# Optimization experiments

Measured on AMD Instinct MI355X. Metric: run time of the kernel, lower is better.

## Reference

```python
import jax, jax.numpy as jnp
import numpy as np

TAU = 2.0      # LIF membrane time constant (spikingjelly default-style, decay_input=True)
VTH = 0.5      # v_threshold from init
S = 4          # time_steps
EPS = 1e-5     # BatchNorm eps
ALPHA = 4.0    # surrogate sigmoid alpha (spikingjelly Sigmoid default)

@jax.custom_vjp
def spike(x):
    # Heaviside forward (spikingjelly: x >= 0 -> 1)
    return (x >= 0.0).astype(x.dtype)

def _spike_fwd(x):
    return spike(x), x

def _spike_bwd(x, g):
    sg = jax.nn.sigmoid(ALPHA * x)
    return (g * ALPHA * sg * (1.0 - sg),)

spike.defvjp(_spike_fwd, _spike_bwd)

def bn(y, gamma, beta, mean, var):
    # inference-mode BatchNorm2d over channel axis 1; y: (B, C, T, V)
    inv = gamma * jax.lax.rsqrt(var + EPS)
    return y * inv[None, :, None, None] + (beta - mean * inv)[None, :, None, None]


def setup_inputs() -> dict:
    key = jax.random.key(0)
    ks = jax.random.split(key, 16)
    B, T, C, V, H, NC = 16, 512, 3, 16, 128, 12
    inp = {
        "x": jax.random.normal(ks[0], (B, T, C, V), dtype=jnp.float32),
        "w1": jax.random.normal(ks[1], (H, C), dtype=jnp.float32) * (1.0 / np.sqrt(C)),
        "b1": jax.random.normal(ks[2], (H,), dtype=jnp.float32) * 0.01,
        "g1": jnp.ones((H,), jnp.float32),
        "be1": jnp.zeros((H,), jnp.float32),
        "m1": jax.random.normal(ks[3], (H,), dtype=jnp.float32) * 0.1,
        "rv1": jax.random.uniform(ks[4], (H,), dtype=jnp.float32) + 0.5,
        "w2": jax.random.normal(ks[5], (H, H), dtype=jnp.float32) * (1.0 / np.sqrt(H)),
        "b2": jax.random.normal(ks[6], (H,), dtype=jnp.float32) * 0.01,
        "g2": jnp.ones((H,), jnp.float32),
        "be2": jnp.zeros((H,), jnp.float32),
        "m2": jax.random.normal(ks[7], (H,), dtype=jnp.float32) * 0.1,
        "rv2": jax.random.uniform(ks[8], (H,), dtype=jnp.float32) + 0.5,
        "wc": jax.random.normal(ks[9], (NC, H), dtype=jnp.float32) * (1.0 / np.sqrt(H)),
        "bc": jax.random.normal(ks[10], (NC,), dtype=jnp.float32) * 0.01,
    }
    return inp


def reference(x, w1, b1, g1, be1, m1, rv1, w2, b2, g2, be2, m2, rv2, wc, bc):
    # x: (B, T, C, V) -> channels-first (B, C, T, V) as in torch permute
    xc = jnp.transpose(x, (0, 2, 1, 3))
    # fc1 1x1 conv + BN; input identical across all S steps, so compute once
    h1 = bn(jnp.einsum('bctv,oc->botv', xc, w1) + b1[None, :, None, None],
            g1, be1, m1, rv1)  # (B, H, T, V)

    def step(carry, _):
        v1s, v2s, acc = carry
        # LIF1: decay_input=True, v_reset=0 hard reset
        v1n = v1s + (h1 - v1s) / TAU
        s1 = spike(v1n - VTH)
        v1n = v1n * (1.0 - s1)
        # fc2 1x1 conv + BN on spikes
        h2 = bn(jnp.einsum('botv,po->bptv', s1, w2) + b2[None, :, None, None],
                g2, be2, m2, rv2)
        # LIF2
        v2n = v2s + (h2 - v2s) / TAU
        s2 = spike(v2n - VTH)
        v2n = v2n * (1.0 - s2)
        return (v1n, v2n, acc + s2), None

    z = jnp.zeros_like(h1)
    (_, _, acc), _ = jax.lax.scan(step, (z, z, z), None, length=S)
    # mean over S, then mean over T and V -> (B, H); dropout is identity in eval
    feat = (acc / S).mean(axis=(2, 3))
    return feat @ wc.T + bc
```

## Files before the change

kernel.cpp:

```cpp
#include <hip/hip_runtime.h>
#include <hip/hip_bf16.h>
#include <stdint.h>
#include <math.h>

#define B_ 16
#define T_ 512
#define V_ 16
#define H_ 128
#define NC_ 12

typedef float v2f __attribute__((ext_vector_type(2)));
typedef __attribute__((ext_vector_type(8))) short s8frag;
typedef __attribute__((ext_vector_type(16))) float f16frag;
typedef unsigned long long u64;


__device__ __forceinline__ unsigned short bf16_rne(float w) {
    unsigned u = __float_as_uint(w);
    unsigned r = (u + 0x7FFFu + ((u >> 16) & 1u)) >> 16;
    return (unsigned short)r;
}
__device__ __forceinline__ float bf16_f32(unsigned short h) {
    return __uint_as_float((unsigned)h << 16);
}
__device__ __forceinline__ void split8(const float* __restrict__ s, s8frag& hi, s8frag& lo) {
    #pragma unroll
    for (int j = 0; j < 8; ++j) {
        float w = s[j];
        unsigned short hb = bf16_rne(w);
        unsigned short lb = bf16_rne(w - bf16_f32(hb));
        hi[j] = (short)hb;
        lo[j] = (short)lb;
    }
}
__device__ __forceinline__ uint4 expand8(unsigned bt) {
    uint4 r;
    r.x = ((bt      & 1u) * 0x3F80u) | (((bt >> 1) & 1u) * 0x3F800000u);
    r.y = (((bt >> 2) & 1u) * 0x3F80u) | (((bt >> 3) & 1u) * 0x3F800000u);
    r.z = (((bt >> 4) & 1u) * 0x3F80u) | (((bt >> 5) & 1u) * 0x3F800000u);
    r.w = (((bt >> 6) & 1u) * 0x3F80u) | (((bt >> 7) & 1u) * 0x3F800000u);
    return r;
}

#define ROUNDS 8
__global__ __launch_bounds__(256, 3) void snn_main(
    const float* __restrict__ x,
    const float* __restrict__ w1, const float* __restrict__ b1,
    const float* __restrict__ g1, const float* __restrict__ be1,
    const float* __restrict__ m1, const float* __restrict__ rv1,
    const float* __restrict__ w2, const float* __restrict__ b2,
    const float* __restrict__ g2, const float* __restrict__ be2,
    const float* __restrict__ m2, const float* __restrict__ rv2,
    float* __restrict__ feat)
{
    __shared__ uint4 afrag[2][2][8][64];
    __shared__ uint4 msk[4][16];

    const int tid  = threadIdx.x;
    const int lane = tid & 63;
    const int wv   = tid >> 6;
    const int nl   = lane & 15;
    const int kg   = (lane >> 4) & 1;
    const int ch4  = lane >> 5;
    const int bb   = blockIdx.x >> 6;
    const int sbase = (blockIdx.x & 63) * (ROUNDS * 16);

    const int p = lane, q = lane + 64;
    v2f w0v = { w1[p*3+0], w1[q*3+0] };
    v2f w1v = { w1[p*3+1], w1[q*3+1] };
    v2f w2v = { w1[p*3+2], w1[q*3+2] };
    v2f b1v = { b1[p], b1[q] };
    float i1a = g1[p] * (float)(1.0 / sqrt((double)(rv1[p] + 1e-5f)));
    float i1b = g1[q] * (float)(1.0 / sqrt((double)(rv1[q] + 1e-5f)));
    v2f i1v = { i1a, i1b };
    v2f d1v = { be1[p] - m1[p] * i1a, be1[q] - m1[q] * i1b };

    const int chn = wv * 32 + (lane & 31);
    float i2c = g2[chn] * (float)(1.0 / sqrt((double)(rv2[chn] + 1e-5f)));
    float d2c = be2[chn] - m2[chn] * i2c;
    float b2c = b2[chn];

    s8frag bh[8], bl[8];
    #pragma unroll
    for (int c = 0; c < 8; ++c)
        split8(&w2[chn * H_ + c * 16 + ch4 * 8], bh[c], bl[c]);

    float facc = 0.f;

    #define CONSUME(BUF)                                                        \
        for (int tt = 0; tt < 2; ++tt) {                                        \
            f16frag acch = {0.f,0.f,0.f,0.f,0.f,0.f,0.f,0.f,                    \
                            0.f,0.f,0.f,0.f,0.f,0.f,0.f,0.f};                   \
            f16frag accl = acch;                                                \
            _Pragma("unroll")                                                   \
            for (int c = 0; c < 8; ++c) {                                       \
                s8frag a = *(const s8frag*)&afrag[BUF][tt][c][lane];            \
                acch = __builtin_amdgcn_mfma_f32_32x32x16_bf16(a, bh[c], acch, 0,0,0); \
                accl = __builtin_amdgcn_mfma_f32_32x32x16_bf16(a, bl[c], accl, 0,0,0); \
            }                                                                   \
            f16frag accs = acch + accl;                                         \
            _Pragma("unroll")                                                   \
            for (int g = 0; g < 4; ++g) {                                       \
                float v = 0.f;                                                  \
                _Pragma("unroll")                                               \
                for (int s = 0; s < 4; ++s) {                                   \
                    float h2 = (accs[g*4+s] + b2c) * i2c + d2c;                 \
                    v = v + (h2 - v) * 0.5f;                                    \
                    bool sp = v >= 0.5f;                                        \
                    v = sp ? 0.f : v;                                           \
                    facc += sp ? 1.f : 0.f;                                     \
                }                                                               \
            }                                                                   \
        }

    for (int r = 0; r < ROUNDS; ++r) {
        #pragma unroll
        for (int i = 0; i < 4; ++i) {
            int site = sbase + r * 16 + wv * 4 + i;
            int t = site >> 4, v = site & 15;
            const float* xp = x + ((size_t)(bb * T_ + t) * 3) * V_ + v;
            float x0 = xp[0], x1 = xp[V_], x2 = xp[2 * V_];

            v2f h1 = ((x0 * w0v + x1 * w1v + x2 * w2v) + b1v) * i1v + d1v;
            v2f v1t = h1 * 0.5f;
            v2f v2t = v1t + h1 * 0.25f;
            v2f v3t = v2t + (h1 - v2t) * 0.5f;
            v2f v4t = v3t + (h1 - v3t) * 0.5f;

            u64 t1a = __ballot(v1t.x >= 0.5f), t2a = __ballot(v2t.x >= 0.5f);
            u64 t3a = __ballot(v3t.x >= 0.5f), t4a = __ballot(v4t.x >= 0.5f);
            u64 t1b = __ballot(v1t.y >= 0.5f), t2b = __ballot(v2t.y >= 0.5f);
            u64 t3b = __ballot(v3t.y >= 0.5f), t4b = __ballot(v4t.y >= 0.5f);
            u64 s3a = t1a | (t3a & ~t2a), s3b = t1b | (t3b & ~t2b);
            u64 s4a = t2a | (t4a & ~t3a), s4b = t2b | (t4b & ~t3b);

            u64 mx = (lane == 0) ? t1a : (lane == 1) ? t2a : (lane == 2) ? s3a : s4a;
            u64 my = (lane == 0) ? t1b : (lane == 1) ? t2b : (lane == 2) ? s3b : s4b;
            if (lane < 4) {
                uint4 mm;
                mm.x = (unsigned)mx; mm.y = (unsigned)(mx >> 32);
                mm.z = (unsigned)my; mm.w = (unsigned)(my >> 32);
                msk[wv][i * 4 + lane] = mm;
            }
        }
        {
            uint4 mm = msk[wv][nl];
            u64 wsel = ch4 ? ((u64)mm.z | ((u64)mm.w << 32))
                           : ((u64)mm.x | ((u64)mm.y << 32));
            int tt   = wv >> 1;
            int slot = ((wv & 1) * 16 + nl) + 32 * kg;
            int buf  = r & 1;
            #pragma unroll
            for (int j = 0; j < 4; ++j) {
                unsigned by = (unsigned)(wsel >> (kg * 8 + j * 16)) & 0xFFu;
                afrag[buf][tt][ch4 * 4 + j][slot] = expand8(by);
            }
        }
        if (r > 0) { int pb = (r - 1) & 1; CONSUME(pb); }
        __syncthreads();
    }
    { int pb = (ROUNDS - 1) & 1; CONSUME(pb); }
    #undef CONSUME

    facc += __shfl_xor(facc, 32);
    if (lane < 32) atomicAdd(&feat[bb * H_ + chn], facc);
}

__global__ __launch_bounds__(128) void classifier_kernel(
    const float* __restrict__ feat,
    const float* __restrict__ wc,
    const float* __restrict__ bc,
    float* __restrict__ out) {
    __shared__ float fb[H_];
    int b = blockIdx.x, t = threadIdx.x;
    fb[t] = feat[b * H_ + t] * (1.0f / 32768.0f);
    __syncthreads();
    if (t < NC_) {
        float s = 0.f;
        for (int h = 0; h < H_; ++h) s += fb[h] * wc[t * H_ + h];
        out[b * NC_ + t] = s + bc[t];
    }
}

extern "C" void kernel_launch(void* const* d_in, const int* in_sizes, int n_in,
                              void* d_out, int out_size, void* d_ws, size_t ws_size,
                              hipStream_t stream) {
    const float* x   = (const float*)d_in[0];
    const float* w1  = (const float*)d_in[1];
    const float* b1  = (const float*)d_in[2];
    const float* g1  = (const float*)d_in[3];
    const float* be1 = (const float*)d_in[4];
    const float* m1  = (const float*)d_in[5];
    const float* rv1 = (const float*)d_in[6];
    const float* w2  = (const float*)d_in[7];
    const float* b2  = (const float*)d_in[8];
    const float* g2  = (const float*)d_in[9];
    const float* be2 = (const float*)d_in[10];
    const float* m2  = (const float*)d_in[11];
    const float* rv2 = (const float*)d_in[12];
    const float* wc  = (const float*)d_in[13];
    const float* bc  = (const float*)d_in[14];

    float* feat = (float*)d_ws;
    float* out  = (float*)d_out;

    snn_main<<<1024, 256, 0, stream>>>(x, w1, b1, g1, be1, m1, rv1,
                                       w2, b2, g2, be2, m2, rv2, feat);
    classifier_kernel<<<B_, 128, 0, stream>>>(feat, wc, bc, out);
}
```

Before: 141.5 us.

## Make each wave self-contained: per-wave spike masks, no block barriers, folded BN

```diff
diff --git a/kernel.cpp b/kernel.cpp
--- a/kernel.cpp
+++ b/kernel.cpp
@@ -23,10 +23,11 @@
 __device__ __forceinline__ float bf16_f32(unsigned short h) {
     return __uint_as_float((unsigned)h << 16);
 }
-__device__ __forceinline__ void split8(const float* __restrict__ s, s8frag& hi, s8frag& lo) {
+__device__ __forceinline__ void split8s(const float* __restrict__ s, float scale,
+                                        s8frag& hi, s8frag& lo) {
     #pragma unroll
     for (int j = 0; j < 8; ++j) {
-        float w = s[j];
+        float w = s[j] * scale;
         unsigned short hb = bf16_rne(w);
         unsigned short lb = bf16_rne(w - bf16_f32(hb));
         hi[j] = (short)hb;
@@ -42,8 +43,8 @@
     return r;
 }
 
-#define ROUNDS 8
-__global__ __launch_bounds__(256, 3) void snn_main(
+#define TILES 16
+__global__ __launch_bounds__(256) void snn_main(
     const float* __restrict__ x,
     const float* __restrict__ w1, const float* __restrict__ b1,
     const float* __restrict__ g1, const float* __restrict__ be1,
@@ -53,17 +54,14 @@
     const float* __restrict__ m2, const float* __restrict__ rv2,
     float* __restrict__ feat)
 {
-    __shared__ uint4 afrag[2][2][8][64];
-    __shared__ uint4 msk[4][16];
+    __shared__ u64 msk[4][64];
 
     const int tid  = threadIdx.x;
     const int lane = tid & 63;
     const int wv   = tid >> 6;
-    const int nl   = lane & 15;
-    const int kg   = (lane >> 4) & 1;
-    const int ch4  = lane >> 5;
+    const int hl5  = lane >> 5;
     const int bb   = blockIdx.x >> 6;
-    const int sbase = (blockIdx.x & 63) * (ROUNDS * 16);
+    const int sbase = (blockIdx.x & 63) * (TILES * 8);
 
     const int p = lane, q = lane + 64;
     v2f w0v = { w1[p*3+0], w1[q*3+0] };
@@ -78,45 +76,22 @@
     const int chn = wv * 32 + (lane & 31);
     float i2c = g2[chn] * (float)(1.0 / sqrt((double)(rv2[chn] + 1e-5f)));
     float d2c = be2[chn] - m2[chn] * i2c;
-    float b2c = b2[chn];
+    float e2  = b2[chn] * i2c + d2c;
 
     s8frag bh[8], bl[8];
     #pragma unroll
     for (int c = 0; c < 8; ++c)
-        split8(&w2[chn * H_ + c * 16 + ch4 * 8], bh[c], bl[c]);
+        split8s(&w2[chn * H_ + c * 16 + hl5 * 8], i2c, bh[c], bl[c]);
+
+    const int si = (lane & 31) >> 2;
+    const int st = lane & 3;
 
     float facc = 0.f;
 
-    #define CONSUME(BUF)                                                        \
-        for (int tt = 0; tt < 2; ++tt) {                                        \
-            f16frag acch = {0.f,0.f,0.f,0.f,0.f,0.f,0.f,0.f,                    \
-                            0.f,0.f,0.f,0.f,0.f,0.f,0.f,0.f};                   \
-            f16frag accl = acch;                                                \
-            _Pragma("unroll")                                                   \
-            for (int c = 0; c < 8; ++c) {                                       \
-                s8frag a = *(const s8frag*)&afrag[BUF][tt][c][lane];            \
-                acch = __builtin_amdgcn_mfma_f32_32x32x16_bf16(a, bh[c], acch, 0,0,0); \
-                accl = __builtin_amdgcn_mfma_f32_32x32x16_bf16(a, bl[c], accl, 0,0,0); \
-            }                                                                   \
-            f16frag accs = acch + accl;                                         \
-            _Pragma("unroll")                                                   \
-            for (int g = 0; g < 4; ++g) {                                       \
-                float v = 0.f;                                                  \
-                _Pragma("unroll")                                               \
-                for (int s = 0; s < 4; ++s) {                                   \
-                    float h2 = (accs[g*4+s] + b2c) * i2c + d2c;                 \
-                    v = v + (h2 - v) * 0.5f;                                    \
-                    bool sp = v >= 0.5f;                                        \
-                    v = sp ? 0.f : v;                                           \
-                    facc += sp ? 1.f : 0.f;                                     \
-                }                                                               \
-            }                                                                   \
-        }
-
-    for (int r = 0; r < ROUNDS; ++r) {
+    for (int tt = 0; tt < TILES; ++tt) {
         #pragma unroll
-        for (int i = 0; i < 4; ++i) {
-            int site = sbase + r * 16 + wv * 4 + i;
+        for (int i = 0; i < 8; ++i) {
+            int site = sbase + tt * 8 + i;
             int t = site >> 4, v = site & 15;
             const float* xp = x + ((size_t)(bb * T_ + t) * 3) * V_ + v;
             float x0 = xp[0], x1 = xp[V_], x2 = xp[2 * V_];
@@ -134,33 +109,45 @@
             u64 s3a = t1a | (t3a & ~t2a), s3b = t1b | (t3b & ~t2b);
             u64 s4a = t2a | (t4a & ~t3a), s4b = t2b | (t4b & ~t3b);
 
-            u64 mx = (lane == 0) ? t1a : (lane == 1) ? t2a : (lane == 2) ? s3a : s4a;
-            u64 my = (lane == 0) ? t1b : (lane == 1) ? t2b : (lane == 2) ? s3b : s4b;
-            if (lane < 4) {
-                uint4 mm;
-                mm.x = (unsigned)mx; mm.y = (unsigned)(mx >> 32);
-                mm.z = (unsigned)my; mm.w = (unsigned)(my >> 32);
-                msk[wv][i * 4 + lane] = mm;
+            u64 mA = (lane == 0) ? t1a : (lane == 2) ? t2a : (lane == 4) ? s3a : s4a;
+            u64 mB = (lane == 1) ? t1b : (lane == 3) ? t2b : (lane == 5) ? s3b : s4b;
+            if (lane < 8) {
+                msk[wv][i * 8 + lane] = (lane & 1) ? mB : mA;
             }
         }
-        {
-            uint4 mm = msk[wv][nl];
-            u64 wsel = ch4 ? ((u64)mm.z | ((u64)mm.w << 32))
-                           : ((u64)mm.x | ((u64)mm.y << 32));
-            int tt   = wv >> 1;
-            int slot = ((wv & 1) * 16 + nl) + 32 * kg;
-            int buf  = r & 1;
+        __builtin_amdgcn_wave_barrier();
+
+        u64 m0 = msk[wv][si * 8 + st * 2 + 0];
+        u64 m1 = msk[wv][si * 8 + st * 2 + 1];
+
+        f16frag acch = { e2,e2,e2,e2,e2,e2,e2,e2,e2,e2,e2,e2,e2,e2,e2,e2 };
+        f16frag accl = { 0.f,0.f,0.f,0.f,0.f,0.f,0.f,0.f,
+                         0.f,0.f,0.f,0.f,0.f,0.f,0.f,0.f };
+        #pragma unroll
+        for (int c = 0; c < 8; ++c) {
+            u64 src = (c < 4) ? m0 : m1;
+            unsigned by = (unsigned)(src >> (((c & 3) * 2 + hl5) * 8)) & 0xFFu;
+            uint4 fr = expand8(by);
+            s8frag a;
+            ((uint4*)&a)[0] = fr;
+            acch = __builtin_amdgcn_mfma_f32_32x32x16_bf16(a, bh[c], acch, 0, 0, 0);
+            accl = __builtin_amdgcn_mfma_f32_32x32x16_bf16(a, bl[c], accl, 0, 0, 0);
+        }
+        f16frag accs = acch + accl;
+
+        #pragma unroll
+        for (int g = 0; g < 4; ++g) {
+            float v = 0.f;
             #pragma unroll
-            for (int j = 0; j < 4; ++j) {
-                unsigned by = (unsigned)(wsel >> (kg * 8 + j * 16)) & 0xFFu;
-                afrag[buf][tt][ch4 * 4 + j][slot] = expand8(by);
+            for (int s = 0; s < 4; ++s) {
+                float h2 = accs[g * 4 + s];
+                v = v + (h2 - v) * 0.5f;
+                bool sp = v >= 0.5f;
+                v = sp ? 0.f : v;
+                facc += sp ? 1.f : 0.f;
             }
         }
-        if (r > 0) { int pb = (r - 1) & 1; CONSUME(pb); }
-        __syncthreads();
     }
-    { int pb = (ROUNDS - 1) & 1; CONSUME(pb); }
-    #undef CONSUME
 
     facc += __shfl_xor(facc, 32);
     if (lane < 32) atomicAdd(&feat[bb * H_ + chn], facc);
```

Result: slower. 215.3 us (+52.2%).
